# Kernel tuning notes

Measured on AMD Instinct MI355X. Metric: run time of the kernel, lower is better.

## Reference

```python
import math
import jax, jax.numpy as jnp
import numpy as np

B, L, C, H = 2, 2048, 1024, 16
D = C // H


def new_gelu(x):
    return 0.5 * x * (1.0 + jnp.tanh(math.sqrt(2.0 / math.pi) * (x + 0.044715 * x ** 3)))


def layer_norm(x, w, b, eps=1e-5):
    mu = jnp.mean(x, axis=-1, keepdims=True)
    var = jnp.var(x, axis=-1, keepdims=True)
    return (x - mu) * jax.lax.rsqrt(var + eps) * w + b


def setup_inputs() -> dict:
    key = jax.random.key(0)
    ks = jax.random.split(key, 8)
    s = 0.02
    return {
        "x": jax.random.normal(ks[0], (B, L, C), dtype=jnp.float32),
        "ln1_w": jnp.ones((C,), jnp.float32),
        "ln1_b": jnp.zeros((C,), jnp.float32),
        "w_attn": jax.random.normal(ks[1], (C, 3 * C), dtype=jnp.float32) * s,
        "b_attn": jnp.zeros((3 * C,), jnp.float32),
        "w_proj": jax.random.normal(ks[2], (C, C), dtype=jnp.float32) * s,
        "b_proj": jnp.zeros((C,), jnp.float32),
        "ln2_w": jnp.ones((C,), jnp.float32),
        "ln2_b": jnp.zeros((C,), jnp.float32),
        "w_fc": jax.random.normal(ks[3], (C, 4 * C), dtype=jnp.float32) * s,
        "b_fc": jnp.zeros((4 * C,), jnp.float32),
        "w_fc2": jax.random.normal(ks[4], (4 * C, C), dtype=jnp.float32) * s,
        "b_fc2": jnp.zeros((C,), jnp.float32),
    }


def reference(x, ln1_w, ln1_b, w_attn, b_attn, w_proj, b_proj,
              ln2_w, ln2_b, w_fc, b_fc, w_fc2, b_fc2):
    # --- self-attention sublayer (pre-LN) ---
    h = layer_norm(x, ln1_w, ln1_b)
    qkv = h @ w_attn + b_attn                              # [B, L, 3C]
    q, k, v = jnp.split(qkv, 3, axis=-1)
    q = q.reshape(B, L, H, D)
    k = k.reshape(B, L, H, D)
    v = v.reshape(B, L, H, D)
    att = jnp.einsum("bqhd,bkhd->bhqk", q, k) * (1.0 / math.sqrt(D))
    causal = jnp.tril(jnp.ones((L, L), dtype=bool))
    att = jnp.where(causal[None, None], att, -jnp.inf)
    att = jax.nn.softmax(att, axis=-1)
    y = jnp.einsum("bhqk,bkhd->bqhd", att, v).reshape(B, L, C)
    y = y @ w_proj + b_proj
    x = x + y
    # --- MLP sublayer (pre-LN) ---
    h = layer_norm(x, ln2_w, ln2_b)
    h = new_gelu(h @ w_fc + b_fc)
    h = h @ w_fc2 + b_fc2
    return x + h
```

## Files before the change

kernel.cpp:

```cpp
#include <hip/hip_runtime.h>
#include <math.h>

#define B_ 2
#define L_ 2048
#define C_ 1024
#define H_ 16
#define M_ (B_*L_)

typedef short s16x8 __attribute__((ext_vector_type(8)));
typedef float f32x4 __attribute__((ext_vector_type(4)));

__device__ __forceinline__ unsigned short f2bf(float f) {
    unsigned int u = __float_as_uint(f);
    u += 0x7fffu + ((u >> 16) & 1u);
    return (unsigned short)(u >> 16);
}

__device__ __forceinline__ float fexp2(float x) {
#if __has_builtin(__builtin_amdgcn_exp2f)
    return __builtin_amdgcn_exp2f(x);
#else
    return exp2f(x);
#endif
}

__device__ __forceinline__ float frcp(float x) {
#if __has_builtin(__builtin_amdgcn_rcpf)
    return __builtin_amdgcn_rcpf(x);
#else
    return 1.0f / x;
#endif
}

__device__ __forceinline__ void gl_lds16(const void* g, void* l) {
    __builtin_amdgcn_global_load_lds(
        (const __attribute__((address_space(1))) void*)g,
        (__attribute__((address_space(3))) void*)l, 16, 0, 0);
}

#define VMCNT8() asm volatile("s_waitcnt vmcnt(8)" ::: "memory")
#define VMCNT6() asm volatile("s_waitcnt vmcnt(6)" ::: "memory")
#define VMCNT4() asm volatile("s_waitcnt vmcnt(4)" ::: "memory")
#define VMCNT0() asm volatile("s_waitcnt vmcnt(0)" ::: "memory")
#define LGKM0()  asm volatile("s_waitcnt lgkmcnt(0)" ::: "memory")
#define SCHED0() __builtin_amdgcn_sched_barrier(0)

__device__ __forceinline__ void ln_row(const float* __restrict__ x,
                                       const float* __restrict__ w,
                                       const float* __restrict__ b,
                                       unsigned short* __restrict__ out,
                                       int row, int t,
                                       float* red0, float* red1, float* mv) {
    float4 v = ((const float4*)(x + (size_t)row * C_))[t];
    float s  = v.x + v.y + v.z + v.w;
    float s2 = v.x*v.x + v.y*v.y + v.z*v.z + v.w*v.w;
    #pragma unroll
    for (int off = 32; off > 0; off >>= 1) {
        s  += __shfl_down(s, off);
        s2 += __shfl_down(s2, off);
    }
    int wave = t >> 6, lane = t & 63;
    if (lane == 0) { red0[wave] = s; red1[wave] = s2; }
    __syncthreads();
    if (t == 0) {
        float a = red0[0] + red0[1] + red0[2] + red0[3];
        float c = red1[0] + red1[1] + red1[2] + red1[3];
        float mean = a * (1.0f / C_);
        mv[0] = mean;
        mv[1] = rsqrtf(c * (1.0f / C_) - mean * mean + 1e-5f);
    }
    __syncthreads();
    float mean = mv[0], rstd = mv[1];
    float4 wv = ((const float4*)w)[t];
    float4 bv = ((const float4*)b)[t];
    ushort4 o;
    o.x = f2bf((v.x - mean) * rstd * wv.x + bv.x);
    o.y = f2bf((v.y - mean) * rstd * wv.y + bv.y);
    o.z = f2bf((v.z - mean) * rstd * wv.z + bv.z);
    o.w = f2bf((v.w - mean) * rstd * wv.w + bv.w);
    *(ushort4*)&out[(size_t)row * C_ + t * 4] = o;
}

__global__ __launch_bounds__(256) void ln_bf16(const float* __restrict__ x,
                                               const float* __restrict__ w,
                                               const float* __restrict__ b,
                                               unsigned short* __restrict__ out) {
    __shared__ float red0[4], red1[4], mv[2];
    ln_row(x, w, b, out, blockIdx.x, threadIdx.x, red0, red1, mv);
}

__global__ __launch_bounds__(256) void prep_kernel(
    const float* __restrict__ W0, unsigned short* __restrict__ T0,
    const float* __restrict__ W1, unsigned short* __restrict__ T1,
    const float* __restrict__ W2, unsigned short* __restrict__ T2,
    const float* __restrict__ W3, unsigned short* __restrict__ T3,
    const float* __restrict__ x, const float* __restrict__ lnw,
    const float* __restrict__ lnb, unsigned short* __restrict__ h) {
    __shared__ unsigned short Ts[32][33];
    __shared__ float red0[4], red1[4], mv[2];
    int id = blockIdx.x;
    int t = threadIdx.x;
    if (id >= 12288) {
        ln_row(x, lnw, lnb, h, id - 12288, t, red0, red1, mv);
        return;
    }
    const float* W; unsigned short* WT; int R, C, bx, by;
    if (id < 3072)      { W = W0; WT = T0; R = 1024; C = 3072; bx = id % 96;  by = id / 96; }
    else if (id < 4096) { W = W1; WT = T1; R = 1024; C = 1024; id -= 3072; bx = id & 31;  by = id >> 5; }
    else if (id < 8192) { W = W2; WT = T2; R = 1024; C = 4096; id -= 4096; bx = id & 127; by = id >> 7; }
    else                { W = W3; WT = T3; R = 4096; C = 1024; id -= 8192; bx = id & 31;  by = id >> 5; }
    int tx = t & 31, ty = t >> 5;
    int c0 = bx * 32, r0 = by * 32;
    #pragma unroll
    for (int k = 0; k < 4; ++k)
        Ts[ty + 8*k][tx] = f2bf(W[(size_t)(r0 + ty + 8*k) * C + c0 + tx]);
    __syncthreads();
    #pragma unroll
    for (int k = 0; k < 4; ++k)
        WT[(size_t)(c0 + ty + 8*k) * R + r0 + tx] = Ts[tx][ty + 8*k];
}

__device__ __forceinline__ float gelu_f(float x) {
    float u2 = 1.5957691216057308f * (x + 0.044715f * x * x * x);
    return x * frcp(1.0f + __expf(-u2));
}

template<int ACT, int OBF, int TN, int SC, int KS, int VT, int XS>
__global__ __launch_bounds__(256) void bgemm(const unsigned short* __restrict__ A,
                                             const unsigned short* __restrict__ BT,
                                             const float* __restrict__ bias,
                                             const float* __restrict__ res,
                                             void* __restrict__ Cout,
                                             unsigned short* __restrict__ VtP,
                                             int M, int N, int K) {
    __shared__ __align__(16) unsigned short As[128 * 64];
    __shared__ __align__(16) unsigned short Bs[TN * 64];
    const int t = threadIdx.x, w = t >> 6, quad = (t & 63) >> 4, ln15 = t & 15;
    constexpr int FJ = TN / 32;
    const int woff_m = (w >> 1) * 64, woff_n = (w & 1) * (TN / 2);
    int bxi = blockIdx.x, byi = blockIdx.y;
    if (XS) {
        int id = bxi + (int)gridDim.x * byi;
        int nt = (int)gridDim.x, xcd = id & 7, loc = id >> 3;
        int per = (nt + 7) >> 3;
        bxi = xcd * per + (loc % per);
        byi = loc / per;
        if (bxi >= nt) { bxi = id % nt; byi = id / nt; }
    }
    const int m0g = byi * 128, n0g = bxi * TN;
    f32x4 acc[4][FJ];
    #pragma unroll
    for (int fi = 0; fi < 4; ++fi)
        #pragma unroll
        for (int fj = 0; fj < FJ; ++fj)
            #pragma unroll
            for (int i = 0; i < 4; ++i) acc[fi][fj][i] = 0.0f;

    const int kbeg = (KS > 1) ? (int)blockIdx.z * (K / KS) : 0;
    const int kiters = ((KS > 1) ? K / KS : K) >> 6;

    const unsigned short* ap[4];
    #pragma unroll
    for (int j = 0; j < 4; ++j) {
        int c = j * 256 + t, row = c >> 3, u = (c & 7) ^ (row & 7);
        ap[j] = A + (size_t)(m0g + row) * K + kbeg + u * 8;
    }
    const unsigned short* bp[FJ];
    #pragma unroll
    for (int j = 0; j < FJ; ++j) {
        int c = j * 256 + t, row = c >> 3, u = (c & 7) ^ (row & 7);
        bp[j] = BT + (size_t)(n0g + row) * K + kbeg + u * 8;
    }

    for (int kk = 0; kk < kiters; ++kk) {
        __syncthreads();
        #pragma unroll
        for (int j = 0; j < 4; ++j) {
            gl_lds16(ap[j], As + (j * 256 + w * 64) * 8);
            ap[j] += 64;
        }
        #pragma unroll
        for (int j = 0; j < FJ; ++j) {
            gl_lds16(bp[j], Bs + (j * 256 + w * 64) * 8);
            bp[j] += 64;
        }
        __syncthreads();
        #pragma unroll
        for (int s = 0; s < 2; ++s) {
            s16x8 af[4], bfr[FJ];
            #pragma unroll
            for (int f = 0; f < 4; ++f) {
                int row = woff_m + f * 16 + ln15;
                af[f] = *(const s16x8*)&As[(row * 8 + ((s * 4 + quad) ^ (row & 7))) * 8];
            }
            #pragma unroll
            for (int f = 0; f < FJ; ++f) {
                int row = woff_n + f * 16 + ln15;
                bfr[f] = *(const s16x8*)&Bs[(row * 8 + ((s * 4 + quad) ^ (row & 7))) * 8];
            }
            #pragma unroll
            for (int fi = 0; fi < 4; ++fi)
                #pragma unroll
                for (int fj = 0; fj < FJ; ++fj)
                    acc[fi][fj] = __builtin_amdgcn_mfma_f32_16x16x32_bf16(af[fi], bfr[fj], acc[fi][fj], 0, 0, 0);
        }
    }

    const int colb = n0g + woff_n + ln15;
    if (KS > 1) {
        float* P = (float*)Cout + (size_t)blockIdx.z * M * N;
        #pragma unroll
        for (int fj = 0; fj < FJ; ++fj) {
            const int col = colb + fj * 16;
            #pragma unroll
            for (int fi = 0; fi < 4; ++fi) {
                const int row0 = m0g + woff_m + fi * 16 + quad * 4;
                #pragma unroll
                for (int i = 0; i < 4; ++i)
                    P[(size_t)(row0 + i) * N + col] = acc[fi][fj][i];
            }
        }
        return;
    }
    #pragma unroll
    for (int fj = 0; fj < FJ; ++fj) {
        const int col = colb + fj * 16;
        const float bv = bias[col];
        const float sc = (SC && col < C_) ? 0.18033688011112042f : 1.0f;
        if (VT && col >= 2 * C_) {
            const int vcol = col - 2 * C_;
            #pragma unroll
            for (int fi = 0; fi < 4; ++fi) {
                const int row0 = m0g + woff_m + fi * 16 + quad * 4;
                const int bb = row0 >> 11, l = row0 & (L_ - 1);
                ushort4 pk;
                pk.x = f2bf(acc[fi][fj][0] + bv);
                pk.y = f2bf(acc[fi][fj][1] + bv);
                pk.z = f2bf(acc[fi][fj][2] + bv);
                pk.w = f2bf(acc[fi][fj][3] + bv);
                *(ushort4*)&VtP[(size_t)(bb * 1024 + vcol) * L_ + l] = pk;
            }
        } else {
            #pragma unroll
            for (int fi = 0; fi < 4; ++fi) {
                const int row0 = m0g + woff_m + fi * 16 + quad * 4;
                #pragma unroll
                for (int i = 0; i < 4; ++i) {
                    float v = acc[fi][fj][i] + bv;
                    if (ACT) v = gelu_f(v);
                    if (SC) v *= sc;
                    size_t off = (size_t)(row0 + i) * N + col;
                    if (res != nullptr) v += res[off];
                    if (OBF) ((unsigned short*)Cout)[off] = f2bf(v);
                    else     ((float*)Cout)[off] = v;
                }
            }
        }
    }
}

template<int ACT, int OBF, int BM, int BN, int SC, int KS, int VT, int XS>
__global__ __launch_bounds__(512) void bgemm2(const unsigned short* __restrict__ A,
                                              const unsigned short* __restrict__ BT,
                                              const float* __restrict__ bias,
                                              const float* __restrict__ res,
                                              void* __restrict__ Cout,
                                              unsigned short* __restrict__ VtP,
                                              int M, int N, int K) {
    constexpr int MR = BM / 32;
    constexpr int NR = BN / 64;
    constexpr int WM = BM / 2;
    constexpr int RA = BM / 64;
    constexpr int RB = BN / 64;
    __shared__ __align__(16) unsigned short As[2 * BM * 64];
    __shared__ __align__(16) unsigned short Bs[2 * BN * 64];
    const int t = threadIdx.x, wv = t >> 6, quad = (t & 63) >> 4, ln15 = t & 15;
    const int wm = wv >> 2, wn = wv & 3;
    int bxi = blockIdx.x, byi = blockIdx.y, bzi = blockIdx.z;
    if (XS == 1) {
        int id = bxi + (int)gridDim.x * byi;
        int nt = (int)gridDim.x, xcd = id & 7, loc = id >> 3;
        int per = nt >> 3;
        bxi = xcd * per + (loc % per);
        byi = loc / per;
    } else if (XS == 2) {
        int gx = (int)gridDim.x;
        int id = bxi + gx * byi + (int)(gridDim.x * gridDim.y) * bzi;
        int xcd = id & 7;
        bxi = xcd % gx;
        bzi = xcd / gx;
        byi = id >> 3;
    }
    const int m0g = byi * BM, n0g = bxi * BN;

    f32x4 acc[MR][NR];
    #pragma unroll
    for (int mr = 0; mr < MR; ++mr)
        #pragma unroll
        for (int nr = 0; nr < NR; ++nr)
            #pragma unroll
            for (int i = 0; i < 4; ++i) acc[mr][nr][i] = 0.0f;

    const int kbeg = (KS > 1) ? bzi * (K / KS) : 0;
    const int NT = ((KS > 1) ? K / KS : K) >> 6;

    const unsigned short* ap[RA];
    #pragma unroll
    for (int j = 0; j < RA; ++j) {
        int c = j * 512 + t, row = c >> 3, u = (t & 7) ^ (row & 7);
        ap[j] = A + (size_t)(m0g + row) * K + kbeg + u * 8;
    }
    const unsigned short* bp[RB];
    #pragma unroll
    for (int j = 0; j < RB; ++j) {
        int c = j * 512 + t, row = c >> 3, u = (t & 7) ^ (row & 7);
        bp[j] = BT + (size_t)(n0g + row) * K + kbeg + u * 8;
    }

    auto STAGE = [&](int kt, int buf) {
        unsigned short* Ad = As + buf * (BM * 64);
        unsigned short* Bd = Bs + buf * (BN * 64);
        #pragma unroll
        for (int j = 0; j < RA; ++j)
            gl_lds16(ap[j] + (size_t)kt * 64, Ad + (j * 512 + wv * 64) * 8);
        #pragma unroll
        for (int j = 0; j < RB; ++j)
            gl_lds16(bp[j] + (size_t)kt * 64, Bd + (j * 512 + wv * 64) * 8);
    };

    STAGE(0, 0);
    STAGE(1, 1);
    if constexpr (RA + RB == 8) VMCNT8();
    else if constexpr (RA + RB == 6) VMCNT6();
    else VMCNT4();
    __builtin_amdgcn_s_barrier();

    int buf = 0;
    for (int kt = 0; kt < NT; ++kt) {
        const unsigned short* Ab = As + buf * (BM * 64);
        const unsigned short* Bb = Bs + buf * (BN * 64);
        s16x8 a0[MR], b0[NR], a1[MR], b1[NR];
        #pragma unroll
        for (int mr = 0; mr < MR; ++mr) {
            int row = wm * WM + mr * 16 + ln15;
            a0[mr] = *(const s16x8*)&Ab[(row * 8 + (quad ^ (row & 7))) * 8];
        }
        #pragma unroll
        for (int nr = 0; nr < NR; ++nr) {
            int row = wn * (NR * 16) + nr * 16 + ln15;
            b0[nr] = *(const s16x8*)&Bb[(row * 8 + (quad ^ (row & 7))) * 8];
        }
        #pragma unroll
        for (int mr = 0; mr < MR; ++mr)
            #pragma unroll
            for (int nr = 0; nr < NR; ++nr)
                acc[mr][nr] = __builtin_amdgcn_mfma_f32_16x16x32_bf16(a0[mr], b0[nr], acc[mr][nr], 0, 0, 0);
        #pragma unroll
        for (int mr = 0; mr < MR; ++mr) {
            int row = wm * WM + mr * 16 + ln15;
            a1[mr] = *(const s16x8*)&Ab[(row * 8 + ((4 + quad) ^ (row & 7))) * 8];
        }
        #pragma unroll
        for (int nr = 0; nr < NR; ++nr) {
            int row = wn * (NR * 16) + nr * 16 + ln15;
            b1[nr] = *(const s16x8*)&Bb[(row * 8 + ((4 + quad) ^ (row & 7))) * 8];
        }
        LGKM0();
        __builtin_amdgcn_sched_barrier(0);
        __builtin_amdgcn_s_barrier();
        if (kt + 2 < NT) STAGE(kt + 2, buf);
        __builtin_amdgcn_s_setprio(1);
        #pragma unroll
        for (int mr = 0; mr < MR; ++mr)
            #pragma unroll
            for (int nr = 0; nr < NR; ++nr)
                acc[mr][nr] = __builtin_amdgcn_mfma_f32_16x16x32_bf16(a1[mr], b1[nr], acc[mr][nr], 0, 0, 0);
        __builtin_amdgcn_s_setprio(0);
        if (kt + 2 < NT) {
            if constexpr (RA + RB == 8) VMCNT8();
            else if constexpr (RA + RB == 6) VMCNT6();
            else VMCNT4();
            __builtin_amdgcn_s_barrier();
        } else if (kt + 1 < NT) {
            VMCNT0();
            __builtin_amdgcn_s_barrier();
        }
        buf ^= 1;
    }

    const int colb = n0g + wn * (NR * 16) + ln15;
    if (KS > 1) {
        float* P = (float*)Cout + (size_t)bzi * M * N;
        #pragma unroll
        for (int nr = 0; nr < NR; ++nr) {
            const int col = colb + nr * 16;
            #pragma unroll
            for (int mr = 0; mr < MR; ++mr) {
                const int row0 = m0g + wm * WM + mr * 16 + quad * 4;
                #pragma unroll
                for (int i = 0; i < 4; ++i)
                    P[(size_t)(row0 + i) * N + col] = acc[mr][nr][i];
            }
        }
        return;
    }
    if constexpr (OBF && !VT && BM == 256 && BN == 256) {
        if (res == nullptr) {
            unsigned short* Ep = As;
            unsigned short* Cg = (unsigned short*)Cout;
            #pragma unroll
            for (int half = 0; half < 2; ++half) {
                LGKM0(); __builtin_amdgcn_s_barrier();
                if (wm == half) {
                    #pragma unroll
                    for (int mr = 0; mr < MR; ++mr) {
                        #pragma unroll
                        for (int nr = 0; nr < NR; ++nr) {
                            const int col = wn * 64 + nr * 16 + ln15;
                            const float bv = bias[n0g + col];
                            #pragma unroll
                            for (int i = 0; i < 4; ++i) {
                                const int row = mr * 16 + quad * 4 + i;
                                float v = acc[mr][nr][i] + bv;
                                if (ACT) v = gelu_f(v);
                                if (SC && (n0g + col) < C_) v *= 0.18033688011112042f;
                                Ep[row * 256 + (col ^ (((row >> 2) & 3) << 4))] = f2bf(v);
                            }
                        }
                    }
                }
                LGKM0(); __builtin_amdgcn_s_barrier();
                #pragma unroll
                for (int it = 0; it < 8; ++it) {
                    int off = it * 4096 + t * 8;
                    int row = off >> 8, c0 = off & 255;
                    int sc0 = c0 ^ (((row >> 2) & 3) << 4);
                    s16x8 vld = *(const s16x8*)&Ep[row * 256 + sc0];
                    *(s16x8*)&Cg[(size_t)(m0g + half * 128 + row) * N + n0g + c0] = vld;
                }
            }
            return;
        }
    }
    #pragma unroll
    for (int nr = 0; nr < NR; ++nr) {
        const int col = colb + nr * 16;
        const float bv = bias[col];
        const float sc = (SC && col < C_) ? 0.18033688011112042f : 1.0f;
        if (VT && col >= 2 * C_) {
            const int vcol = col - 2 * C_;
            #pragma unroll
            for (int mr = 0; mr < MR; ++mr) {
                const int row0 = m0g + wm * WM + mr * 16 + quad * 4;
                const int bb = row0 >> 11, l = row0 & (L_ - 1);
                ushort4 pk;
                pk.x = f2bf(acc[mr][nr][0] + bv);
                pk.y = f2bf(acc[mr][nr][1] + bv);
                pk.z = f2bf(acc[mr][nr][2] + bv);
                pk.w = f2bf(acc[mr][nr][3] + bv);
                *(ushort4*)&VtP[(size_t)(bb * 1024 + vcol) * L_ + l] = pk;
            }
        } else {
            #pragma unroll
            for (int mr = 0; mr < MR; ++mr) {
                const int row0 = m0g + wm * WM + mr * 16 + quad * 4;
                #pragma unroll
                for (int i = 0; i < 4; ++i) {
                    float v = acc[mr][nr][i] + bv;
                    if (ACT) v = gelu_f(v);
                    if (SC) v *= sc;
                    size_t off = (size_t)(row0 + i) * N + col;
                    if (res != nullptr) v += res[off];
                    if (OBF) ((unsigned short*)Cout)[off] = f2bf(v);
                    else     ((float*)Cout)[off] = v;
                }
            }
        }
    }
}

__global__ __launch_bounds__(256) void attn_kernel(const unsigned short* __restrict__ qkv,
                                                   const unsigned short* __restrict__ Vt,
                                                   unsigned short* __restrict__ y) {
    __shared__ __align__(16) unsigned short Qs[64 * 64];
    __shared__ __align__(16) unsigned short Ks[2 * 128 * 64];
    __shared__ __align__(16) unsigned short Vs[2 * 64 * 128];
    const int t = threadIdx.x, w = t >> 6, quad = (t & 63) >> 4, ln15 = t & 15;
    const int wq = w >> 1, wk = w & 1;
    const int id = blockIdx.x;
    const int bh = (id & 7) * 4 + ((id >> 3) & 3);
    const int qpair = id >> 5;
    const int b = bh >> 4, h = bh & 15;

    #pragma unroll 1
    for (int rep = 0; rep < 2; ++rep) {
        const int qt = rep == 0 ? (31 - qpair) : qpair;
        const int q0 = qt * 64;
        if (rep) __syncthreads();
        #pragma unroll
        for (int j = 0; j < 2; ++j) {
            int c = j * 256 + t;
            int row = c >> 3, u = (c & 7) ^ (row & 7);
            gl_lds16(qkv + (size_t)(b * L_ + q0 + row) * (3*C_) + h * 64 + u * 8,
                     Qs + (j * 256 + w * 64) * 8);
        }
        #pragma unroll
        for (int j = 0; j < 4; ++j) {
            int c = j * 256 + t;
            int row = c >> 3, u = (c & 7) ^ (row & 7);
            gl_lds16(qkv + (size_t)(b * L_ + row) * (3*C_) + C_ + h * 64 + u * 8,
                     Ks + (j * 256 + w * 64) * 8);
        }
        #pragma unroll
        for (int j = 0; j < 4; ++j) {
            int c = j * 256 + t;
            int row = c >> 4, u = (c & 15) ^ (row & 15);
            gl_lds16(Vt + (size_t)(bh * 64 + row) * L_ + u * 8,
                     Vs + (j * 256 + w * 64) * 8);
        }
        __syncthreads();

        s16x8 qb[2][2];
        #pragma unroll
        for (int qf = 0; qf < 2; ++qf) {
            int row = wq * 32 + qf * 16 + ln15;
            #pragma unroll
            for (int s = 0; s < 2; ++s)
                qb[qf][s] = *(const s16x8*)&Qs[row * 64 + (((s * 4 + quad)) ^ (row & 7)) * 8];
        }

        f32x4 O[4][2];
        float m_[2] = {-INFINITY, -INFINITY}, l_[2] = {0.0f, 0.0f};
        #pragma unroll
        for (int df = 0; df < 4; ++df)
            #pragma unroll
            for (int qf = 0; qf < 2; ++qf)
                #pragma unroll
                for (int i = 0; i < 4; ++i) O[df][qf][i] = 0.0f;

        const int nkt = (qt >> 1) + 1;
        int buf = 0;
        for (int kt = 0; kt < nkt; ++kt) {
            unsigned short* Kb = Ks + buf * (128 * 64);
            unsigned short* Vb = Vs + buf * (64 * 128);
            unsigned short* Kn = Ks + (buf ^ 1) * (128 * 64);
            unsigned short* Vn = Vs + (buf ^ 1) * (64 * 128);
            if (kt + 1 < nkt) {
                #pragma unroll
                for (int j = 0; j < 4; ++j) {
                    int c = j * 256 + t;
                    int row = c >> 3, u = (c & 7) ^ (row & 7);
                    gl_lds16(qkv + (size_t)(b * L_ + (kt + 1) * 128 + row) * (3*C_) + C_ + h * 64 + u * 8,
                             Kn + (j * 256 + w * 64) * 8);
                }
                #pragma unroll
                for (int j = 0; j < 4; ++j) {
                    int c = j * 256 + t;
                    int row = c >> 4, u = (c & 15) ^ (row & 15);
                    gl_lds16(Vt + (size_t)(bh * 64 + row) * L_ + (kt + 1) * 128 + u * 8,
                             Vn + (j * 256 + w * 64) * 8);
                }
            }

            f32x4 St[2][4];
            #pragma unroll
            for (int qf = 0; qf < 2; ++qf)
                #pragma unroll
                for (int kf = 0; kf < 4; ++kf)
                    #pragma unroll
                    for (int i = 0; i < 4; ++i) St[qf][kf][i] = 0.0f;
            #pragma unroll
            for (int s = 0; s < 2; ++s) {
                s16x8 ka[4];
                #pragma unroll
                for (int kf = 0; kf < 4; ++kf) {
                    int row = wk * 64 + kf * 16 + ln15;
                    ka[kf] = *(const s16x8*)&Kb[row * 64 + ((s * 4 + quad) ^ (row & 7)) * 8];
                }
                #pragma unroll
                for (int qf = 0; qf < 2; ++qf)
                    #pragma unroll
                    for (int kf = 0; kf < 4; ++kf)
                        St[qf][kf] = __builtin_amdgcn_mfma_f32_16x16x32_bf16(ka[kf], qb[qf][s], St[qf][kf], 0, 0, 0);
            }
            LGKM0(); SCHED0();
            __builtin_amdgcn_s_barrier();
            SCHED0();

            unsigned short* Pw = Kb + w * 2048;
            const bool diag = (kt == nkt - 1);
            #pragma unroll
            for (int qf = 0; qf < 2; ++qf) {
                const int qg = q0 + wq * 32 + qf * 16 + ln15;
                float mt = -INFINITY;
                if (diag) {
                    #pragma unroll
                    for (int kf = 0; kf < 4; ++kf)
                        #pragma unroll
                        for (int i = 0; i < 4; ++i) {
                            int key = kt * 128 + wk * 64 + kf * 16 + quad * 4 + i;
                            float sv = St[qf][kf][i];
                            sv = (key > qg) ? -INFINITY : sv;
                            St[qf][kf][i] = sv;
                            mt = fmaxf(mt, sv);
                        }
                } else {
                    #pragma unroll
                    for (int kf = 0; kf < 4; ++kf)
                        #pragma unroll
                        for (int i = 0; i < 4; ++i) mt = fmaxf(mt, St[qf][kf][i]);
                }
                mt = fmaxf(mt, __shfl_xor(mt, 16));
                mt = fmaxf(mt, __shfl_xor(mt, 32));
                float ms;
                if (__all(mt <= m_[qf] + 8.0f && m_[qf] > -INFINITY)) {
                    ms = m_[qf];
                } else {
                    const float mn = fmaxf(m_[qf], mt);
                    ms = (mn == -INFINITY) ? 0.0f : mn;
                    const float alpha = fexp2(m_[qf] - ms);
                    l_[qf] *= alpha;
                    m_[qf] = mn;
                    #pragma unroll
                    for (int df = 0; df < 4; ++df) O[df][qf] *= alpha;
                }
                float rs = 0.0f;
                #pragma unroll
                for (int kf = 0; kf < 4; ++kf)
                    #pragma unroll
                    for (int i = 0; i < 4; ++i) {
                        float e = fexp2(St[qf][kf][i] - ms);
                        St[qf][kf][i] = e;
                        rs += e;
                    }
                rs += __shfl_xor(rs, 16);
                rs += __shfl_xor(rs, 32);
                l_[qf] += rs;
                #pragma unroll
                for (int kf = 0; kf < 4; ++kf) {
                    int row = qf * 16 + ln15;
                    int slot = (kf * 2 + (quad >> 1)) ^ (row & 7);
                    unsigned u0 = __float_as_uint(St[qf][kf][0]) + 0x8000u;
                    unsigned u1 = __float_as_uint(St[qf][kf][1]) + 0x8000u;
                    unsigned u2 = __float_as_uint(St[qf][kf][2]) + 0x8000u;
                    unsigned u3 = __float_as_uint(St[qf][kf][3]) + 0x8000u;
                    uint2 pk;
                    pk.x = __builtin_amdgcn_perm(u1, u0, 0x07060302u);
                    pk.y = __builtin_amdgcn_perm(u3, u2, 0x07060302u);
                    *(uint2*)&Pw[row * 64 + slot * 8 + (quad & 1) * 4] = pk;
                }
            }

            #pragma unroll
            for (int s2 = 0; s2 < 2; ++s2) {
                s16x8 pb[2], va[4];
                #pragma unroll
                for (int qf = 0; qf < 2; ++qf) {
                    int row = qf * 16 + ln15;
                    pb[qf] = *(const s16x8*)&Pw[row * 64 + ((s2 * 4 + quad) ^ (row & 7)) * 8];
                }
                #pragma unroll
                for (int df = 0; df < 4; ++df) {
                    int row = df * 16 + ln15;
                    int uu = wk * 8 + s2 * 4 + quad;
                    va[df] = *(const s16x8*)&Vb[row * 128 + (uu ^ (row & 15)) * 8];
                }
                #pragma unroll
                for (int df = 0; df < 4; ++df)
                    #pragma unroll
                    for (int qf = 0; qf < 2; ++qf)
                        O[df][qf] = __builtin_amdgcn_mfma_f32_16x16x32_bf16(va[df], pb[qf], O[df][qf], 0, 0, 0);
            }

            if (kt + 1 < nkt) {
                LGKM0(); VMCNT0(); SCHED0();
                __builtin_amdgcn_s_barrier();
                SCHED0();
            }
            buf ^= 1;
        }

        __syncthreads();
        float* OB  = (float*)Ks;
        float* MLm = (float*)Qs;
        float* MLl = MLm + 64;
        if (wk == 1) {
            #pragma unroll
            for (int qf = 0; qf < 2; ++qf) {
                int rq = wq * 32 + qf * 16 + ln15;
                if (quad == 0) { MLm[rq] = m_[qf]; MLl[rq] = l_[qf]; }
                #pragma unroll
                for (int df = 0; df < 4; ++df) {
                    float4 o;
                    o.x = O[df][qf][0]; o.y = O[df][qf][1]; o.z = O[df][qf][2]; o.w = O[df][qf][3];
                    *(float4*)&OB[rq * 64 + (((df * 4 + quad) ^ (rq & 15)) << 2)] = o;
                }
            }
        }
        __syncthreads();
        if (wk == 0) {
            #pragma unroll
            for (int qf = 0; qf < 2; ++qf) {
                const int rq = wq * 32 + qf * 16 + ln15;
                const float m1 = MLm[rq], l1 = MLl[rq];
                const float mF = fmaxf(m_[qf], m1);
                float e0 = fexp2(m_[qf] - mF);
                float e1 = (m1 == -INFINITY) ? 0.0f : fexp2(m1 - mF);
                const float linv = frcp(l_[qf] * e0 + l1 * e1);
                e0 *= linv; e1 *= linv;
                #pragma unroll
                for (int df = 0; df < 4; ++df) {
                    float4 o1 = *(const float4*)&OB[rq * 64 + (((df * 4 + quad) ^ (rq & 15)) << 2)];
                    ushort4 yv;
                    yv.x = f2bf(O[df][qf][0] * e0 + o1.x * e1);
                    yv.y = f2bf(O[df][qf][1] * e0 + o1.y * e1);
                    yv.z = f2bf(O[df][qf][2] * e0 + o1.z * e1);
                    yv.w = f2bf(O[df][qf][3] * e0 + o1.w * e1);
                    *(ushort4*)&y[(size_t)(b * L_ + q0 + rq) * C_ + h * 64 + df * 16 + quad * 4] = yv;
                }
            }
        }
    }
}

#define MB(x) ((size_t)(x) << 20)

extern "C" void kernel_launch(void* const* d_in, const int* in_sizes, int n_in,
                              void* d_out, int out_size, void* d_ws, size_t ws_size,
                              hipStream_t stream) {
    const float* x      = (const float*)d_in[0];
    const float* ln1_w  = (const float*)d_in[1];
    const float* ln1_b  = (const float*)d_in[2];
    const float* w_attn = (const float*)d_in[3];
    const float* b_attn = (const float*)d_in[4];
    const float* w_proj = (const float*)d_in[5];
    const float* b_proj = (const float*)d_in[6];
    const float* ln2_w  = (const float*)d_in[7];
    const float* ln2_b  = (const float*)d_in[8];
    const float* w_fc   = (const float*)d_in[9];
    const float* b_fc   = (const float*)d_in[10];
    const float* w_fc2  = (const float*)d_in[11];
    const float* b_fc2  = (const float*)d_in[12];
    float* out = (float*)d_out;

    char* ws = (char*)d_ws;
    unsigned short* wT1  = (unsigned short*)(ws + MB(0));
    unsigned short* wT2  = (unsigned short*)(ws + MB(6));
    unsigned short* wT3  = (unsigned short*)(ws + MB(8));
    unsigned short* wT4  = (unsigned short*)(ws + MB(16));
    unsigned short* h_bf = (unsigned short*)(ws + MB(24));
    unsigned short* qkv  = (unsigned short*)(ws + MB(32));
    unsigned short* Vt   = (unsigned short*)(ws + MB(56));
    unsigned short* y_bf = (unsigned short*)(ws + MB(64));
    float*          x1   = (float*)(ws + MB(72));
    unsigned short* f_bf = (unsigned short*)(ws + MB(88));
    dim3 b256(256), b512(512);

    prep_kernel<<<12288 + M_, b256, 0, stream>>>(w_attn, wT1, w_proj, wT2,
                                                 w_fc, wT3, w_fc2, wT4,
                                                 x, ln1_w, ln1_b, h_bf);
    bgemm<0,1,128,1,1,1,0><<<dim3(3*C_/128, M_/128), b256, 0, stream>>>(
        h_bf, wT1, b_attn, nullptr, qkv, Vt, M_, 3*C_, C_);
    attn_kernel<<<512, b256, 0, stream>>>(qkv, Vt, y_bf);
    bgemm<0,0,64,0,1,0,0><<<dim3(C_/64, M_/128), b256, 0, stream>>>(
        y_bf, wT2, b_proj, x, x1, nullptr, M_, C_, C_);
    ln_bf16<<<M_, b256, 0, stream>>>(x1, ln2_w, ln2_b, h_bf);
    bgemm2<1,1,256,256,0,1,0,1><<<dim3(4*C_/256, M_/256), b512, 0, stream>>>(
        h_bf, wT3, b_fc, nullptr, f_bf, nullptr, M_, 4*C_, C_);
    bgemm2<0,0,128,128,0,1,0,1><<<dim3(C_/128, M_/128), b512, 0, stream>>>(
        f_bf, wT4, b_fc2, x1, out, nullptr, M_, C_, 4*C_);
}
```

Before: 351.4 us.

## Double-buffer bgemm LDS loads and split-K the final MLP GEMM

The simple bgemm kernel now keeps two LDS stages and issues the next tile's global-to-LDS loads while the MFMAs for the current tile run. It also replaces the single-sync-per-step loop with vmcnt waits and barriers. Separately, the fc2 GEMM now uses split-K=2 with a 128x256 tile writing fp32 partials, and a new combine kernel adds the partials, bias and residual. This trades an extra pass over partial buffers for more parallelism in the long-K GEMM, and doubles the LDS use of bgemm.

```diff
diff --git a/kernel.cpp b/kernel.cpp
--- a/kernel.cpp
+++ b/kernel.cpp
@@ -133,10 +133,10 @@
                                              void* __restrict__ Cout,
                                              unsigned short* __restrict__ VtP,
                                              int M, int N, int K) {
-    __shared__ __align__(16) unsigned short As[128 * 64];
-    __shared__ __align__(16) unsigned short Bs[TN * 64];
+    constexpr int FJ = TN / 32;
+    __shared__ __align__(16) unsigned short As[2 * 128 * 64];
+    __shared__ __align__(16) unsigned short Bs[2 * TN * 64];
     const int t = threadIdx.x, w = t >> 6, quad = (t & 63) >> 4, ln15 = t & 15;
-    constexpr int FJ = TN / 32;
     const int woff_m = (w >> 1) * 64, woff_n = (w & 1) * (TN / 2);
     int bxi = blockIdx.x, byi = blockIdx.y;
     if (XS) {
@@ -157,7 +157,7 @@
             for (int i = 0; i < 4; ++i) acc[fi][fj][i] = 0.0f;
 
     const int kbeg = (KS > 1) ? (int)blockIdx.z * (K / KS) : 0;
-    const int kiters = ((KS > 1) ? K / KS : K) >> 6;
+    const int NT = ((KS > 1) ? K / KS : K) >> 6;
 
     const unsigned short* ap[4];
     #pragma unroll
@@ -172,38 +172,71 @@
         bp[j] = BT + (size_t)(n0g + row) * K + kbeg + u * 8;
     }
 
-    for (int kk = 0; kk < kiters; ++kk) {
-        __syncthreads();
-        #pragma unroll
-        for (int j = 0; j < 4; ++j) {
-            gl_lds16(ap[j], As + (j * 256 + w * 64) * 8);
-            ap[j] += 64;
-        }
-        #pragma unroll
-        for (int j = 0; j < FJ; ++j) {
-            gl_lds16(bp[j], Bs + (j * 256 + w * 64) * 8);
-            bp[j] += 64;
-        }
-        __syncthreads();
-        #pragma unroll
-        for (int s = 0; s < 2; ++s) {
-            s16x8 af[4], bfr[FJ];
-            #pragma unroll
-            for (int f = 0; f < 4; ++f) {
-                int row = woff_m + f * 16 + ln15;
-                af[f] = *(const s16x8*)&As[(row * 8 + ((s * 4 + quad) ^ (row & 7))) * 8];
-            }
-            #pragma unroll
-            for (int f = 0; f < FJ; ++f) {
-                int row = woff_n + f * 16 + ln15;
-                bfr[f] = *(const s16x8*)&Bs[(row * 8 + ((s * 4 + quad) ^ (row & 7))) * 8];
-            }
-            #pragma unroll
-            for (int fi = 0; fi < 4; ++fi)
-                #pragma unroll
-                for (int fj = 0; fj < FJ; ++fj)
-                    acc[fi][fj] = __builtin_amdgcn_mfma_f32_16x16x32_bf16(af[fi], bfr[fj], acc[fi][fj], 0, 0, 0);
-        }
+    auto STAGE = [&](int kt, int buf) {
+        unsigned short* Ad = As + buf * (128 * 64);
+        unsigned short* Bd = Bs + buf * (TN * 64);
+        #pragma unroll
+        for (int j = 0; j < 4; ++j)
+            gl_lds16(ap[j] + (size_t)kt * 64, Ad + (j * 256 + w * 64) * 8);
+        #pragma unroll
+        for (int j = 0; j < FJ; ++j)
+            gl_lds16(bp[j] + (size_t)kt * 64, Bd + (j * 256 + w * 64) * 8);
+    };
+
+    STAGE(0, 0);
+    STAGE(1, 1);
+    if constexpr (4 + FJ == 8) VMCNT8(); else VMCNT6();
+    __builtin_amdgcn_s_barrier();
+
+    int buf = 0;
+    for (int kk = 0; kk < NT; ++kk) {
+        const unsigned short* Ab = As + buf * (128 * 64);
+        const unsigned short* Bb = Bs + buf * (TN * 64);
+        s16x8 a0[4], b0[FJ], a1[4], b1[FJ];
+        #pragma unroll
+        for (int f = 0; f < 4; ++f) {
+            int row = woff_m + f * 16 + ln15;
+            a0[f] = *(const s16x8*)&Ab[(row * 8 + (quad ^ (row & 7))) * 8];
+        }
+        #pragma unroll
+        for (int f = 0; f < FJ; ++f) {
+            int row = woff_n + f * 16 + ln15;
+            b0[f] = *(const s16x8*)&Bb[(row * 8 + (quad ^ (row & 7))) * 8];
+        }
+        #pragma unroll
+        for (int fi = 0; fi < 4; ++fi)
+            #pragma unroll
+            for (int fj = 0; fj < FJ; ++fj)
+                acc[fi][fj] = __builtin_amdgcn_mfma_f32_16x16x32_bf16(a0[fi], b0[fj], acc[fi][fj], 0, 0, 0);
+        #pragma unroll
+        for (int f = 0; f < 4; ++f) {
+            int row = woff_m + f * 16 + ln15;
+            a1[f] = *(const s16x8*)&Ab[(row * 8 + ((4 + quad) ^ (row & 7))) * 8];
+        }
+        #pragma unroll
+        for (int f = 0; f < FJ; ++f) {
+            int row = woff_n + f * 16 + ln15;
+            b1[f] = *(const s16x8*)&Bb[(row * 8 + ((4 + quad) ^ (row & 7))) * 8];
+        }
+        LGKM0();
+        SCHED0();
+        __builtin_amdgcn_s_barrier();
+        if (kk + 2 < NT) STAGE(kk + 2, buf);
+        __builtin_amdgcn_s_setprio(1);
+        #pragma unroll
+        for (int fi = 0; fi < 4; ++fi)
+            #pragma unroll
+            for (int fj = 0; fj < FJ; ++fj)
+                acc[fi][fj] = __builtin_amdgcn_mfma_f32_16x16x32_bf16(a1[fi], b1[fj], acc[fi][fj], 0, 0, 0);
+        __builtin_amdgcn_s_setprio(0);
+        if (kk + 2 < NT) {
+            if constexpr (4 + FJ == 8) VMCNT8(); else VMCNT6();
+            __builtin_amdgcn_s_barrier();
+        } else if (kk + 1 < NT) {
+            VMCNT0();
+            __builtin_amdgcn_s_barrier();
+        }
+        buf ^= 1;
     }
 
     const int colb = n0g + woff_n + ln15;
@@ -479,6 +512,24 @@
     }
 }
 
+__global__ __launch_bounds__(256) void combine_out(const float* __restrict__ p,
+                                                   const float* __restrict__ bias,
+                                                   const float* __restrict__ res,
+                                                   float* __restrict__ out) {
+    int idx = blockIdx.x * 256 + threadIdx.x;
+    size_t off = (size_t)idx * 4;
+    float4 a = *(const float4*)&p[off];
+    float4 b = *(const float4*)&p[(size_t)M_ * C_ + off];
+    float4 r = *(const float4*)&res[off];
+    float4 bb = *(const float4*)&bias[off & (C_ - 1)];
+    float4 o;
+    o.x = a.x + b.x + r.x + bb.x;
+    o.y = a.y + b.y + r.y + bb.y;
+    o.z = a.z + b.z + r.z + bb.z;
+    o.w = a.w + b.w + r.w + bb.w;
+    *(float4*)&out[off] = o;
+}
+
 __global__ __launch_bounds__(256) void attn_kernel(const unsigned short* __restrict__ qkv,
                                                    const unsigned short* __restrict__ Vt,
                                                    unsigned short* __restrict__ y) {
@@ -754,6 +805,7 @@
     unsigned short* y_bf = (unsigned short*)(ws + MB(64));
     float*          x1   = (float*)(ws + MB(72));
     unsigned short* f_bf = (unsigned short*)(ws + MB(88));
+    float*          part = (float*)(ws + MB(32));
     dim3 b256(256), b512(512);
 
     prep_kernel<<<12288 + M_, b256, 0, stream>>>(w_attn, wT1, w_proj, wT2,
@@ -767,6 +819,7 @@
     ln_bf16<<<M_, b256, 0, stream>>>(x1, ln2_w, ln2_b, h_bf);
     bgemm2<1,1,256,256,0,1,0,1><<<dim3(4*C_/256, M_/256), b512, 0, stream>>>(
         h_bf, wT3, b_fc, nullptr, f_bf, nullptr, M_, 4*C_, C_);
-    bgemm2<0,0,128,128,0,1,0,1><<<dim3(C_/128, M_/128), b512, 0, stream>>>(
-        f_bf, wT4, b_fc2, x1, out, nullptr, M_, C_, 4*C_);
-}
+    bgemm2<0,0,128,256,0,2,0,2><<<dim3(C_/256, M_/128, 2), b512, 0, stream>>>(
+        f_bf, wT4, nullptr, nullptr, part, nullptr, M_, C_, 4*C_);
+    combine_out<<<(M_*C_)/(4*256), b256, 0, stream>>>(part, b_fc2, x1, out);
+}
```

After: 350.0 us. About the same (-0.4%).
